# Kernel tuning notes

Hardware: AMD Instinct MI355X
Metric: run time of the kernel (lower is better)

The kernel has to match this reference:

```python
import jax, jax.numpy as jnp
import numpy as np

D_FEAT, HID, N_LAYERS = 6, 64, 2
NEG_SLOPE = 0.01


def gru_layer(x_seq, W_ih, W_hh, b_ih, b_hh):
    # x_seq: [T, N, in]; PyTorch gate order r, z, n
    N = x_seq.shape[1]
    h0 = jnp.zeros((N, W_hh.shape[1]), x_seq.dtype)
    def step(h, x_t):
        gi = x_t @ W_ih.T + b_ih
        gh = h @ W_hh.T + b_hh
        i_r, i_z, i_n = jnp.split(gi, 3, axis=-1)
        h_r, h_z, h_n = jnp.split(gh, 3, axis=-1)
        r = jax.nn.sigmoid(i_r + h_r)
        z = jax.nn.sigmoid(i_z + h_z)
        n = jnp.tanh(i_n + r * h_n)
        h_new = (1.0 - z) * n + z * h
        return h_new, h_new
    _, ys = jax.lax.scan(step, h0, x_seq)
    return ys  # [T, N, H]


def setup_inputs() -> dict:
    key = jax.random.key(0)
    ks = jax.random.split(key, 16)
    N, T = 4000, 60
    x = jax.random.normal(ks[0], (N, D_FEAT * T), dtype=jnp.float32)
    relation_matrix = jax.random.randint(ks[1], (N, N, 8), 0, 2).astype(jnp.float32)
    s = 0.1
    p = {
        'W_ih0': jax.random.normal(ks[2], (3 * HID, D_FEAT), jnp.float32) * s,
        'W_hh0': jax.random.normal(ks[3], (3 * HID, HID), jnp.float32) * s,
        'b_ih0': jnp.zeros((3 * HID,), jnp.float32),
        'b_hh0': jnp.zeros((3 * HID,), jnp.float32),
        'W_ih1': jax.random.normal(ks[4], (3 * HID, HID), jnp.float32) * s,
        'W_hh1': jax.random.normal(ks[5], (3 * HID, HID), jnp.float32) * s,
        'b_ih1': jnp.zeros((3 * HID,), jnp.float32),
        'b_hh1': jnp.zeros((3 * HID,), jnp.float32),
        'W_0': jax.random.normal(ks[6], (2 * HID, 1), jnp.float32) * s,
        'b_0': jnp.zeros((), jnp.float32),
        'W_1': jax.random.normal(ks[7], (2 * HID, 1), jnp.float32) * s,
        'b_1': jnp.zeros((), jnp.float32),
        'W_2': jax.random.normal(ks[8], (2 * HID, 1), jnp.float32) * s,
        'b_2': jnp.zeros((), jnp.float32),
        'fc_w': jax.random.normal(ks[9], (1, 2 * HID), jnp.float32) * s,
        'fc_b': jnp.zeros((1,), jnp.float32),
    }
    return dict(x=x, relation_matrix=relation_matrix, **p)


def _head_softmax(h, W, b, mask):
    # weight[i,j] = leaky_relu(h_i @ W[:H] + h_j @ W[H:] + b); avoids [N,N,2H] concat
    H = h.shape[1]
    a = h @ W[:H]            # [N,1]
    c = h @ W[H:]            # [N,1]
    w = jax.nn.leaky_relu(a + c.T + b, NEG_SLOPE)  # [N,N]
    valid = jnp.where(mask == 0, -1000000.0, mask * w)
    return jax.nn.softmax(valid, axis=1)


def reference(x, relation_matrix, W_ih0, W_hh0, b_ih0, b_hh0, W_ih1, W_hh1, b_ih1, b_hh1,
              W_0, b_0, W_1, b_1, W_2, b_2, fc_w, fc_b):
    N = x.shape[0]
    xs = x.reshape(N, D_FEAT, -1).transpose(2, 0, 1)  # [T, N, d_feat]
    y1 = gru_layer(xs, W_ih0, W_hh0, b_ih0, b_hh0)
    y2 = gru_layer(y1, W_ih1, W_hh1, b_ih1, b_hh1)
    h = y2[-1]  # [N, H] last time step
    mask = jnp.sum(relation_matrix, axis=2)  # [N, N]
    s0 = _head_softmax(h, W_0, b_0, mask)
    s1 = _head_softmax(h, W_1, b_1, mask)
    s2 = _head_softmax(h, W_2, b_2, mask)
    agg = ((s0 + s1 + s2) / 3.0) @ h  # [N, H]
    hid = jnp.concatenate([h, agg], axis=1)  # [N, 2H]
    pred = (hid @ fc_w.T + fc_b).squeeze(-1)  # [N]
    return pred
```

## Files before the change

kernel.cpp:

```cpp
#include <hip/hip_runtime.h>

typedef __attribute__((ext_vector_type(8))) short bf16x8;
typedef __attribute__((ext_vector_type(4))) float f32x4;
typedef __attribute__((ext_vector_type(4))) float f4v;

__device__ __forceinline__ unsigned short f2bf(float f){
  unsigned u = __builtin_bit_cast(unsigned, f);
  u += 0x7FFFu + ((u >> 16) & 1u);
  return (unsigned short)(u >> 16);
}
__device__ __forceinline__ float bf2f(unsigned short b){
  unsigned u = ((unsigned)b) << 16;
  return __builtin_bit_cast(float, u);
}
__device__ __forceinline__ float sigmoidf_(float x){ return 1.f/(1.f + __expf(-x)); }
__device__ __forceinline__ float tanhf_(float x){
  float a = fabsf(x);
  float t = __expf(-2.f*a);
  float r = (1.f - t)/(1.f + t);
  return copysignf(r, x);
}

struct WF { bf16x8 hi, lo; };

__device__ __forceinline__ void mmsplit(bf16x8 ah, bf16x8 al, const WF& B,
                                        f32x4& Dh, f32x4& Dl){
  Dh = __builtin_amdgcn_mfma_f32_16x16x32_bf16(ah, B.hi, Dh, 0, 0, 0);
  Dl = __builtin_amdgcn_mfma_f32_16x16x32_bf16(al, B.hi, Dl, 0, 0, 0);
  Dl = __builtin_amdgcn_mfma_f32_16x16x32_bf16(ah, B.lo, Dl, 0, 0, 0);
}

__device__ __forceinline__ WF load_wf(const float* W, int ldk, int row, int k0, int kmax){
  WF f;
  #pragma unroll
  for (int j = 0; j < 8; j++){
    int k = k0 + j;
    float v = (k < kmax) ? W[row*ldk + k] : 0.f;
    unsigned short hb = f2bf(v);
    f.hi[j] = (short)hb;
    f.lo[j] = (short)f2bf(v - bf2f(hb));
  }
  return f;
}

__global__ __launch_bounds__(512, 2)
void gru_kernel(const float* __restrict__ x,
                const float* __restrict__ Wih0, const float* __restrict__ Whh0,
                const float* __restrict__ bih0, const float* __restrict__ bhh0,
                const float* __restrict__ Wih1, const float* __restrict__ Whh1,
                const float* __restrict__ bih1, const float* __restrict__ bhh1,
                const float* __restrict__ W0h, const float* __restrict__ W1h,
                const float* __restrict__ W2h,
                const float* __restrict__ fcw, const float* __restrict__ fcb,
                float* __restrict__ ac){
  __shared__ unsigned short xp_hi[16][60][8];
  __shared__ unsigned short xp_lo[16][60][8];
  __shared__ unsigned short h0hi[2][16][72], h0lo[2][16][72];
  __shared__ unsigned short h1hi[2][16][72], h1lo[2][16][72];
  __shared__ float hsh[16][64];

  const int tid  = threadIdx.x;
  const int lane = tid & 63;
  const int wv   = tid >> 6;
  const bool isA = (wv < 4);
  const int w    = wv & 3;
  const int c    = lane & 15;
  const int q    = lane >> 4;
  const int d    = w*16 + c;
  const int nbase = blockIdx.x * 16;

  for (int v = tid; v < 16*360; v += 512){
    int n = v / 360, rem = v % 360;
    int dd = rem / 60, tt = rem % 60;
    float f = x[(size_t)(nbase + n)*360 + rem];
    unsigned short hb = f2bf(f);
    xp_hi[n][tt][dd] = hb;
    xp_lo[n][tt][dd] = f2bf(f - bf2f(hb));
  }
  for (int v = tid; v < 16*60*2; v += 512){
    int n = v / 120, rem = v % 120;
    int tt = rem >> 1, dd = 6 + (rem & 1);
    xp_hi[n][tt][dd] = 0; xp_lo[n][tt][dd] = 0;
  }
  for (int v = tid; v < 2*16*72; v += 512){
    ((unsigned short*)h0hi)[v] = 0; ((unsigned short*)h0lo)[v] = 0;
    ((unsigned short*)h1hi)[v] = 0; ((unsigned short*)h1lo)[v] = 0;
  }

  const float* bib = isA ? bih0 : bih1;
  const float* bhb = isA ? bhh0 : bhh1;
  const float bir = bib[d], biz = bib[64+d], bin = bib[128+d];
  const float bhr = bhb[d], bhz = bhb[64+d], bhn = bhb[128+d];

  WF Bu[3][2], Bv[3][2];
  #pragma unroll
  for (int g = 0; g < 3; g++){
    int row = g*64 + d;
    if (isA){
      Bu[g][0] = load_wf(Wih0, 6, row, q*8, 6);
      Bu[g][1] = Bu[g][0];
      #pragma unroll
      for (int kt = 0; kt < 2; kt++)
        Bv[g][kt] = load_wf(Whh0, 64, row, kt*32 + q*8, 64);
    } else {
      #pragma unroll
      for (int kt = 0; kt < 2; kt++){
        Bu[g][kt] = load_wf(Wih1, 64, row, kt*32 + q*8, 64);
        Bv[g][kt] = load_wf(Whh1, 64, row, kt*32 + q*8, 64);
      }
    }
  }

  float hold[4] = {0,0,0,0};

  auto stepB = [&](int s){
    const int rb = (s + 1) & 1;
    const int sb = s & 1;
    bf16x8 ayh[2], ayl[2], ahh[2], ahl[2];
    #pragma unroll
    for (int kt = 0; kt < 2; kt++){
      ayh[kt] = *(const bf16x8*)&h0hi[rb][c][kt*32 + q*8];
      ayl[kt] = *(const bf16x8*)&h0lo[rb][c][kt*32 + q*8];
      ahh[kt] = *(const bf16x8*)&h1hi[sb][c][kt*32 + q*8];
      ahl[kt] = *(const bf16x8*)&h1lo[sb][c][kt*32 + q*8];
    }
    f32x4 RH = {0,0,0,0}, RL = {0,0,0,0};
    f32x4 ZH = {0,0,0,0}, ZL = {0,0,0,0};
    f32x4 NIH = {0,0,0,0}, NIL = {0,0,0,0};
    f32x4 NHH = {0,0,0,0}, NHL = {0,0,0,0};
    #pragma unroll
    for (int kt = 0; kt < 2; kt++){
      mmsplit(ayh[kt], ayl[kt], Bu[0][kt], RH, RL);
      mmsplit(ayh[kt], ayl[kt], Bu[1][kt], ZH, ZL);
      mmsplit(ayh[kt], ayl[kt], Bu[2][kt], NIH, NIL);
      mmsplit(ahh[kt], ahl[kt], Bv[0][kt], RH, RL);
      mmsplit(ahh[kt], ahl[kt], Bv[1][kt], ZH, ZL);
      mmsplit(ahh[kt], ahl[kt], Bv[2][kt], NHH, NHL);
    }
    #pragma unroll
    for (int rI = 0; rI < 4; rI++){
      float rv = sigmoidf_(RH[rI] + RL[rI] + bir + bhr);
      float zv = sigmoidf_(ZH[rI] + ZL[rI] + biz + bhz);
      float nv = tanhf_(NIH[rI] + NIL[rI] + bin + rv*(NHH[rI] + NHL[rI] + bhn));
      float hnew = (1.f - zv)*nv + zv*hold[rI];
      hold[rI] = hnew;
      unsigned short hb = f2bf(hnew);
      int node = q*4 + rI;
      h1hi[rb][node][d] = hb;
      h1lo[rb][node][d] = f2bf(hnew - bf2f(hb));
    }
  };

  __syncthreads();

  #pragma unroll 1
  for (int t = 0; t < 60; t++){
    if (isA){
      const int p  = t & 1;
      const int nb = p ^ 1;
      bf16x8 ah[2], al[2];
      #pragma unroll
      for (int kt = 0; kt < 2; kt++){
        ah[kt] = *(const bf16x8*)&h0hi[p][c][kt*32 + q*8];
        al[kt] = *(const bf16x8*)&h0lo[p][c][kt*32 + q*8];
      }
      bf16x8 axh = {}, axl = {};
      if (q == 0){
        axh = *(const bf16x8*)&xp_hi[c][t][0];
        axl = *(const bf16x8*)&xp_lo[c][t][0];
      }
      f32x4 RH = {0,0,0,0}, RL = {0,0,0,0};
      f32x4 ZH = {0,0,0,0}, ZL = {0,0,0,0};
      f32x4 NIH = {0,0,0,0}, NIL = {0,0,0,0};
      f32x4 NHH = {0,0,0,0}, NHL = {0,0,0,0};
      mmsplit(axh, axl, Bu[0][0], RH, RL);
      mmsplit(axh, axl, Bu[1][0], ZH, ZL);
      mmsplit(axh, axl, Bu[2][0], NIH, NIL);
      #pragma unroll
      for (int kt = 0; kt < 2; kt++){
        mmsplit(ah[kt], al[kt], Bv[0][kt], RH, RL);
        mmsplit(ah[kt], al[kt], Bv[1][kt], ZH, ZL);
        mmsplit(ah[kt], al[kt], Bv[2][kt], NHH, NHL);
      }
      #pragma unroll
      for (int rI = 0; rI < 4; rI++){
        float rv = sigmoidf_(RH[rI] + RL[rI] + bir + bhr);
        float zv = sigmoidf_(ZH[rI] + ZL[rI] + biz + bhz);
        float nv = tanhf_(NIH[rI] + NIL[rI] + bin + rv*(NHH[rI] + NHL[rI] + bhn));
        float hnew = (1.f - zv)*nv + zv*hold[rI];
        hold[rI] = hnew;
        unsigned short hb = f2bf(hnew);
        int node = q*4 + rI;
        h0hi[nb][node][d] = hb;
        h0lo[nb][node][d] = f2bf(hnew - bf2f(hb));
      }
    } else if (t > 0){
      stepB(t - 1);
    }
    __syncthreads();
  }

  if (!isA){
    stepB(59);
    #pragma unroll
    for (int rI = 0; rI < 4; rI++)
      hsh[q*4 + rI][d] = hold[rI];
  }
  __syncthreads();

  {
    const float w0a = W0h[lane], w0c = W0h[64 + lane];
    const float w1a = W1h[lane], w1c = W1h[64 + lane];
    const float w2a = W2h[lane], w2c = W2h[64 + lane];
    const float gw  = fcw[64 + lane], pw = fcw[lane];
    #pragma unroll
    for (int nn = 0; nn < 2; nn++){
      int n = wv*2 + nn;
      float hv = hsh[n][lane];
      float pa0 = hv*w0a, pc0 = hv*w0c;
      float pa1 = hv*w1a, pc1 = hv*w1c;
      float pa2 = hv*w2a, pc2 = hv*w2c;
      float pg  = hv*gw,  pp  = hv*pw;
      #pragma unroll
      for (int m = 32; m >= 1; m >>= 1){
        pa0 += __shfl_xor(pa0, m, 64); pc0 += __shfl_xor(pc0, m, 64);
        pa1 += __shfl_xor(pa1, m, 64); pc1 += __shfl_xor(pc1, m, 64);
        pa2 += __shfl_xor(pa2, m, 64); pc2 += __shfl_xor(pc2, m, 64);
        pg  += __shfl_xor(pg,  m, 64); pp  += __shfl_xor(pp,  m, 64);
      }
      if (lane == 0){
        size_t node = (size_t)(nbase + n);
        ac[0*4000 + node] = pa0; ac[1*4000 + node] = pc0;
        ac[2*4000 + node] = pa1; ac[3*4000 + node] = pc1;
        ac[4*4000 + node] = pa2; ac[5*4000 + node] = pc2;
        ac[6*4000 + node] = pg;  ac[7*4000 + node] = pp + fcb[0];
      }
    }
  }
}

__global__ __launch_bounds__(256, 4)
void attn2_kernel(const float* __restrict__ rel, const float* __restrict__ ac,
                  const float* __restrict__ b0p, const float* __restrict__ b1p,
                  const float* __restrict__ b2p, float* __restrict__ pred){
  __shared__ float red[4][12];

  const int tid  = threadIdx.x;
  const int lane = tid & 63;
  const int w    = tid >> 6;
  const int i0   = blockIdx.x * 2;
  const float bh[3] = {b0p[0], b1p[0], b2p[0]};

  const float* c0 = ac + (size_t)1*4000;
  const float* c1 = ac + (size_t)3*4000;
  const float* c2 = ac + (size_t)5*4000;
  const float* gv = ac + (size_t)6*4000;
  const float* p0 = ac + (size_t)7*4000;

  float ai[2][3];
  #pragma unroll
  for (int r = 0; r < 2; r++)
    #pragma unroll
    for (int h = 0; h < 3; h++)
      ai[r][h] = ac[(size_t)(2*h)*4000 + i0 + r];

  float z[2][3] = {{0.f,0.f,0.f},{0.f,0.f,0.f}};
  float y[2][3] = {{0.f,0.f,0.f},{0.f,0.f,0.f}};

  {
    const size_t base0 = (size_t)i0*4000;
    const size_t base1 = (size_t)(i0+1)*4000;
    int j = tid;
    bool hv0 = (j < 4000);
    bool hv1 = (j + 256 < 4000);
    f4v a0, a1, a2, a3, b0, b1, b2, b3;
    if (hv0){
      const f4v* rp0 = (const f4v*)(rel + (base0 + j)*8);
      const f4v* rp1 = (const f4v*)(rel + (base1 + j)*8);
      a0 = __builtin_nontemporal_load(rp0);
      a1 = __builtin_nontemporal_load(rp0 + 1);
      a2 = __builtin_nontemporal_load(rp1);
      a3 = __builtin_nontemporal_load(rp1 + 1);
    }
    if (hv1){
      const f4v* rp0 = (const f4v*)(rel + (base0 + j + 256)*8);
      const f4v* rp1 = (const f4v*)(rel + (base1 + j + 256)*8);
      b0 = __builtin_nontemporal_load(rp0);
      b1 = __builtin_nontemporal_load(rp0 + 1);
      b2 = __builtin_nontemporal_load(rp1);
      b3 = __builtin_nontemporal_load(rp1 + 1);
    }
    while (hv0){
      int j2 = j + 512;
      bool hv2 = (j2 < 4000);
      f4v n0, n1, n2, n3;
      if (hv2){
        const f4v* rp0 = (const f4v*)(rel + (base0 + j2)*8);
        const f4v* rp1 = (const f4v*)(rel + (base1 + j2)*8);
        n0 = __builtin_nontemporal_load(rp0);
        n1 = __builtin_nontemporal_load(rp0 + 1);
        n2 = __builtin_nontemporal_load(rp1);
        n3 = __builtin_nontemporal_load(rp1 + 1);
      }
      float mk0 = a0[0]+a0[1]+a0[2]+a0[3] + a1[0]+a1[1]+a1[2]+a1[3];
      float mk1 = a2[0]+a2[1]+a2[2]+a2[3] + a3[0]+a3[1]+a3[2]+a3[3];
      float cv[3] = {c0[j], c1[j], c2[j]};
      float gj = gv[j];
      #pragma unroll
      for (int h = 0; h < 3; h++){
        float s0 = ai[0][h] + cv[h] + bh[h];
        float s1 = ai[1][h] + cv[h] + bh[h];
        float w0 = s0 > 0.f ? s0 : 0.01f*s0;
        float w1 = s1 > 0.f ? s1 : 0.01f*s1;
        float v0 = (mk0 == 0.f) ? -1e6f : mk0*w0;
        float v1 = (mk1 == 0.f) ? -1e6f : mk1*w1;
        float e0 = __expf(v0);
        float e1 = __expf(v1);
        z[0][h] += e0;  y[0][h] = fmaf(e0, gj, y[0][h]);
        z[1][h] += e1;  y[1][h] = fmaf(e1, gj, y[1][h]);
      }
      a0 = b0; a1 = b1; a2 = b2; a3 = b3;
      b0 = n0; b1 = n1; b2 = n2; b3 = n3;
      j += 256; hv0 = hv1; hv1 = hv2;
    }
  }

  #pragma unroll
  for (int r = 0; r < 2; r++)
    #pragma unroll
    for (int h = 0; h < 3; h++){
      float vz = z[r][h], vy = y[r][h];
      #pragma unroll
      for (int m = 32; m >= 1; m >>= 1){
        vz += __shfl_xor(vz, m, 64);
        vy += __shfl_xor(vy, m, 64);
      }
      if (lane == 0){
        red[w][(r*3 + h)*2 + 0] = vz;
        red[w][(r*3 + h)*2 + 1] = vy;
      }
    }
  __syncthreads();
  if (tid < 2){
    int r = tid;
    float acc = 0.f;
    #pragma unroll
    for (int h = 0; h < 3; h++){
      float zz = red[0][(r*3+h)*2] + red[1][(r*3+h)*2] + red[2][(r*3+h)*2] + red[3][(r*3+h)*2];
      float yy = red[0][(r*3+h)*2+1] + red[1][(r*3+h)*2+1] + red[2][(r*3+h)*2+1] + red[3][(r*3+h)*2+1];
      acc += yy / zz;
    }
    pred[i0 + r] = p0[i0 + r] + acc * (1.f/3.f);
  }
}

extern "C" void kernel_launch(void* const* d_in, const int* in_sizes, int n_in,
                              void* d_out, int out_size, void* d_ws, size_t ws_size,
                              hipStream_t stream) {
  const float* x    = (const float*)d_in[0];
  const float* rel  = (const float*)d_in[1];
  const float* Wih0 = (const float*)d_in[2];
  const float* Whh0 = (const float*)d_in[3];
  const float* bih0 = (const float*)d_in[4];
  const float* bhh0 = (const float*)d_in[5];
  const float* Wih1 = (const float*)d_in[6];
  const float* Whh1 = (const float*)d_in[7];
  const float* bih1 = (const float*)d_in[8];
  const float* bhh1 = (const float*)d_in[9];
  const float* W0   = (const float*)d_in[10];
  const float* b0   = (const float*)d_in[11];
  const float* W1   = (const float*)d_in[12];
  const float* b1   = (const float*)d_in[13];
  const float* W2   = (const float*)d_in[14];
  const float* b2   = (const float*)d_in[15];
  const float* fcw  = (const float*)d_in[16];
  const float* fcb  = (const float*)d_in[17];
  float* pred = (float*)d_out;
  float* ac   = (float*)d_ws;

  gru_kernel<<<dim3(250), dim3(512), 0, stream>>>(x, Wih0, Whh0, bih0, bhh0,
                                                  Wih1, Whh1, bih1, bhh1,
                                                  W0, W1, W2, fcw, fcb, ac);
  attn2_kernel<<<dim3(2000), dim3(256), 0, stream>>>(rel, ac, b0, b1, b2, pred);
}
```

Measured before the change: 774.5 us.

## Precompute byte mask for early rows in idle GRU-kernel blocks

Result: slower. 790.1 us (+2.0%).

```diff
diff --git a/kernel.cpp b/kernel.cpp
--- a/kernel.cpp
+++ b/kernel.cpp
@@ -43,8 +43,10 @@
   return f;
 }
 
+#define NPRE 262
+
 __global__ __launch_bounds__(512, 2)
-void gru_kernel(const float* __restrict__ x,
+void gru_kernel(const float* __restrict__ x, const float* __restrict__ rel,
                 const float* __restrict__ Wih0, const float* __restrict__ Whh0,
                 const float* __restrict__ bih0, const float* __restrict__ bhh0,
                 const float* __restrict__ Wih1, const float* __restrict__ Whh1,
@@ -52,7 +54,7 @@
                 const float* __restrict__ W0h, const float* __restrict__ W1h,
                 const float* __restrict__ W2h,
                 const float* __restrict__ fcw, const float* __restrict__ fcb,
-                float* __restrict__ ac){
+                float* __restrict__ ac, unsigned char* __restrict__ mask8){
   __shared__ unsigned short xp_hi[16][60][8];
   __shared__ unsigned short xp_lo[16][60][8];
   __shared__ unsigned short h0hi[2][16][72], h0lo[2][16][72];
@@ -60,6 +62,26 @@
   __shared__ float hsh[16][64];
 
   const int tid  = threadIdx.x;
+
+  if (blockIdx.x >= 250){
+    const int u = blockIdx.x - 250;
+    const size_t r0 = (size_t)(2*u)*4000;
+    const size_t r1 = r0 + 4000;
+    for (int j = tid; j < 4000; j += 512){
+      const f4v* rp0 = (const f4v*)(rel + (r0 + j)*8);
+      const f4v* rp1 = (const f4v*)(rel + (r1 + j)*8);
+      f4v a0 = __builtin_nontemporal_load(rp0);
+      f4v a1 = __builtin_nontemporal_load(rp0 + 1);
+      f4v a2 = __builtin_nontemporal_load(rp1);
+      f4v a3 = __builtin_nontemporal_load(rp1 + 1);
+      float mk0 = a0[0]+a0[1]+a0[2]+a0[3] + a1[0]+a1[1]+a1[2]+a1[3];
+      float mk1 = a2[0]+a2[1]+a2[2]+a2[3] + a3[0]+a3[1]+a3[2]+a3[3];
+      mask8[r0 + j] = (unsigned char)(int)mk0;
+      mask8[r1 + j] = (unsigned char)(int)mk1;
+    }
+    return;
+  }
+
   const int lane = tid & 63;
   const int wv   = tid >> 6;
   const bool isA = (wv < 4);
@@ -240,7 +262,9 @@
 }
 
 __global__ __launch_bounds__(256, 4)
-void attn2_kernel(const float* __restrict__ rel, const float* __restrict__ ac,
+void attn2_kernel(const float* __restrict__ rel,
+                  const unsigned char* __restrict__ mask8,
+                  const float* __restrict__ ac,
                   const float* __restrict__ b0p, const float* __restrict__ b1p,
                   const float* __restrict__ b2p, float* __restrict__ pred){
   __shared__ float red[4][12];
@@ -267,7 +291,33 @@
   float z[2][3] = {{0.f,0.f,0.f},{0.f,0.f,0.f}};
   float y[2][3] = {{0.f,0.f,0.f},{0.f,0.f,0.f}};
 
-  {
+  auto body = [&](float mk0, float mk1, int j){
+    float cv[3] = {c0[j], c1[j], c2[j]};
+    float gj = gv[j];
+    #pragma unroll
+    for (int h = 0; h < 3; h++){
+      float s0 = ai[0][h] + cv[h] + bh[h];
+      float s1 = ai[1][h] + cv[h] + bh[h];
+      float w0 = s0 > 0.f ? s0 : 0.01f*s0;
+      float w1 = s1 > 0.f ? s1 : 0.01f*s1;
+      float v0 = (mk0 == 0.f) ? -1e6f : mk0*w0;
+      float v1 = (mk1 == 0.f) ? -1e6f : mk1*w1;
+      float e0 = __expf(v0);
+      float e1 = __expf(v1);
+      z[0][h] += e0;  y[0][h] = fmaf(e0, gj, y[0][h]);
+      z[1][h] += e1;  y[1][h] = fmaf(e1, gj, y[1][h]);
+    }
+  };
+
+  if (blockIdx.x < NPRE){
+    const size_t m0b = (size_t)i0*4000;
+    const size_t m1b = m0b + 4000;
+    for (int j = tid; j < 4000; j += 256){
+      float mk0 = (float)mask8[m0b + j];
+      float mk1 = (float)mask8[m1b + j];
+      body(mk0, mk1, j);
+    }
+  } else {
     const size_t base0 = (size_t)i0*4000;
     const size_t base1 = (size_t)(i0+1)*4000;
     int j = tid;
@@ -304,21 +354,7 @@
       }
       float mk0 = a0[0]+a0[1]+a0[2]+a0[3] + a1[0]+a1[1]+a1[2]+a1[3];
       float mk1 = a2[0]+a2[1]+a2[2]+a2[3] + a3[0]+a3[1]+a3[2]+a3[3];
-      float cv[3] = {c0[j], c1[j], c2[j]};
-      float gj = gv[j];
-      #pragma unroll
-      for (int h = 0; h < 3; h++){
-        float s0 = ai[0][h] + cv[h] + bh[h];
-        float s1 = ai[1][h] + cv[h] + bh[h];
-        float w0 = s0 > 0.f ? s0 : 0.01f*s0;
-        float w1 = s1 > 0.f ? s1 : 0.01f*s1;
-        float v0 = (mk0 == 0.f) ? -1e6f : mk0*w0;
-        float v1 = (mk1 == 0.f) ? -1e6f : mk1*w1;
-        float e0 = __expf(v0);
-        float e1 = __expf(v1);
-        z[0][h] += e0;  y[0][h] = fmaf(e0, gj, y[0][h]);
-        z[1][h] += e1;  y[1][h] = fmaf(e1, gj, y[1][h]);
-      }
+      body(mk0, mk1, j);
       a0 = b0; a1 = b1; a2 = b2; a3 = b3;
       b0 = n0; b1 = n1; b2 = n2; b3 = n3;
       j += 256; hv0 = hv1; hv1 = hv2;
@@ -377,9 +413,10 @@
   const float* fcb  = (const float*)d_in[17];
   float* pred = (float*)d_out;
   float* ac   = (float*)d_ws;
-
-  gru_kernel<<<dim3(250), dim3(512), 0, stream>>>(x, Wih0, Whh0, bih0, bhh0,
+  unsigned char* mask8 = (unsigned char*)(ac + 8*4000);
+
+  gru_kernel<<<dim3(512), dim3(512), 0, stream>>>(x, rel, Wih0, Whh0, bih0, bhh0,
                                                   Wih1, Whh1, bih1, bhh1,
-                                                  W0, W1, W2, fcw, fcb, ac);
-  attn2_kernel<<<dim3(2000), dim3(256), 0, stream>>>(rel, ac, b0, b1, b2, pred);
-}
+                                                  W0, W1, W2, fcw, fcb, ac, mask8);
+  attn2_kernel<<<dim3(2000), dim3(256), 0, stream>>>(rel, mask8, ac, b0, b1, b2, pred);
+}
```
